# Performance work log

Hardware: AMD Instinct MI355X
Metric: run time of the kernel (lower is better)

## Reference

```python
import jax, jax.numpy as jnp
import numpy as np

V, E, H = 50000, 200, 128
B, R, S, W = 16, 10, 20, 64


def gru_last(x, lengths, Wih, Whh, bih, bhh, reverse=False):
    # x: [N,T,D], lengths: [N] -> final valid hidden state [N,H]
    # Masked-update scan: h only updates on valid timesteps, so after the full
    # scan h equals the packed-sequence final hidden (fwd: t=len-1; bwd: t=0).
    N, T, _ = x.shape
    Hd = Whh.shape[1]
    xi = x @ Wih.T + bih                      # [N,T,3H] input gates, precomputed
    t = jnp.arange(T)
    if reverse:
        xi = xi[:, ::-1]
        valid = (T - 1 - t)[None, :] < lengths[:, None]
    else:
        valid = t[None, :] < lengths[:, None]

    def step(h, inp):
        xg, v = inp
        hg = h @ Whh.T + bhh
        r = jax.nn.sigmoid(xg[:, :Hd] + hg[:, :Hd])
        z = jax.nn.sigmoid(xg[:, Hd:2 * Hd] + hg[:, Hd:2 * Hd])
        n = jnp.tanh(xg[:, 2 * Hd:] + r * hg[:, 2 * Hd:])
        hn = (1.0 - z) * n + z * h
        return jnp.where(v[:, None], hn, h), None

    h0 = jnp.zeros((N, Hd), x.dtype)
    hT, _ = jax.lax.scan(step, h0, (jnp.swapaxes(xi, 0, 1), valid.T))
    return hT


def bigru_last(x, lengths, pf, pb):
    hf = gru_last(x, lengths, *pf, reverse=False)
    hb = gru_last(x, lengths, *pb, reverse=True)
    return 0.5 * (hf + hb)  # reduce bidirectional h_n to hid_dim (mean of dirs)


def setup_inputs() -> dict:
    key = jax.random.key(0)
    ks = jax.random.split(key, 24)

    def gn(k, shape, s=0.1):
        return jax.random.normal(k, shape, dtype=jnp.float32) * s

    return {
        "inputs": jax.random.randint(ks[0], (B, R, S, W), 0, V),
        "sent_lengths": jax.random.randint(ks[1], (B, R, S), 1, W + 1),
        "sent_counts": jax.random.randint(ks[2], (B, R), 1, S + 1),
        "embed": gn(ks[3], (V, E), 1.0),
        "wWih_f": gn(ks[4], (3 * H, E)), "wWhh_f": gn(ks[5], (3 * H, H)),
        "wbih_f": gn(ks[6], (3 * H,)), "wbhh_f": gn(ks[7], (3 * H,)),
        "wWih_b": gn(ks[8], (3 * H, E)), "wWhh_b": gn(ks[9], (3 * H, H)),
        "wbih_b": gn(ks[10], (3 * H,)), "wbhh_b": gn(ks[11], (3 * H,)),
        "sWih_f": gn(ks[12], (3 * H, H)), "sWhh_f": gn(ks[13], (3 * H, H)),
        "sbih_f": gn(ks[14], (3 * H,)), "sbhh_f": gn(ks[15], (3 * H,)),
        "sWih_b": gn(ks[16], (3 * H, H)), "sWhh_b": gn(ks[17], (3 * H, H)),
        "sbih_b": gn(ks[18], (3 * H,)), "sbhh_b": gn(ks[19], (3 * H,)),
        "fc1_w": gn(ks[20], (H // 2, H)), "fc1_b": gn(ks[21], (H // 2,)),
        "fc2_w": gn(ks[22], (1, H // 2)), "fc2_b": gn(ks[23], (1,)),
    }


def reference(inputs, sent_lengths, sent_counts, embed,
              wWih_f, wWhh_f, wbih_f, wbhh_f, wWih_b, wWhh_b, wbih_b, wbhh_b,
              sWih_f, sWhh_f, sbih_f, sbhh_f, sWih_b, sWhh_b, sbih_b, sbhh_b,
              fc1_w, fc1_b, fc2_w, fc2_b):
    b, r, s, w = inputs.shape
    emb = embed[inputs]                                   # [B,R,S,W,E]
    x = emb.reshape(b * r * s, w, -1)
    wlens = sent_lengths.reshape(-1)
    # Word-level BiGRU over all sentences at once (flattened ragged batch)
    sent_rep = bigru_last(x, wlens,
                          (wWih_f, wWhh_f, wbih_f, wbhh_f),
                          (wWih_b, wWhh_b, wbih_b, wbhh_b))  # [B*R*S, H]
    xs = sent_rep.reshape(b * r, s, -1)
    slens = sent_counts.reshape(-1)
    # Sentence-level BiGRU over all reviews at once
    rev = bigru_last(xs, slens,
                     (sWih_f, sWhh_f, sbih_f, sbhh_f),
                     (sWih_b, sWhh_b, sbih_b, sbhh_b)).reshape(b, r, -1)
    h = jax.nn.selu(rev @ fc1_w.T + fc1_b)                # [B,R,H//2]
    r_stars = (h @ fc2_w.T + fc2_b)[..., 0]               # [B,R]
    p_stars = r_stars.mean(-1)                            # [B]
    return p_stars, r_stars
```

## Files before the change

### kernel.cpp

```cpp
#include <hip/hip_runtime.h>
#include <hip/hip_bf16.h>
#include <cstddef>

#define VOCAB 50000
#define EDIM  200
#define HDIM  128
#define BB 16
#define RR 10
#define SS 20
#define WW 64
#define NSENT (BB*RR*SS)
#define NREV  (BB*RR)
#define G3    (3*HDIM)
#define NPROJ (2*G3)

static __device__ __forceinline__ short f2bf(float f) {
    union { float f; unsigned u; } v; v.f = f;
    unsigned r = v.u + 0x7FFFu + ((v.u >> 16) & 1u);
    return (short)(r >> 16);
}
static __device__ __forceinline__ short f2bf_t(float f) {
    union { float f; unsigned u; } v; v.f = f;
    return (short)(v.u >> 16);
}
static __device__ __forceinline__ float bf2f(short s) {
    union { unsigned u; float f; } v;
    v.u = ((unsigned)(unsigned short)s) << 16;
    return v.f;
}
static __device__ __forceinline__ float frcp(float x) {
    return __builtin_amdgcn_rcpf(x);
}
static __device__ __forceinline__ float fsigmoid(float x) {
    return frcp(1.f + __expf(-x));
}
static __device__ __forceinline__ float ftanh(float x) {
    float y = __expf(-2.f * fabsf(x));
    float t = (1.f - y) * frcp(1.f + y);
    return copysignf(t, x);
}

using bf16x8 = __attribute__((ext_vector_type(8))) short;
using f32x4  = __attribute__((ext_vector_type(4))) float;

template<int KREAL, int KPAD>
__global__ __launch_bounds__(256) void preconv(
    const float* __restrict__ A0, int Mreal,
    short* __restrict__ hi, short* __restrict__ lo, int ngroups)
{
    int g = blockIdx.x * 256 + threadIdx.x;
    if (g >= ngroups) return;
    int row = g / (KPAD / 8);
    int k   = (g % (KPAD / 8)) * 8;
    float v[8];
    if (row < Mreal && k < KREAL) {
        const float* p = A0 + (size_t)row * KREAL + k;
        float4 a = *(const float4*)p;
        float4 b = *(const float4*)(p + 4);
        v[0]=a.x; v[1]=a.y; v[2]=a.z; v[3]=a.w;
        v[4]=b.x; v[5]=b.y; v[6]=b.z; v[7]=b.w;
    } else {
        #pragma unroll
        for (int j = 0; j < 8; ++j) v[j] = 0.f;
    }
    bf16x8 h, l;
    #pragma unroll
    for (int j = 0; j < 8; ++j) {
        short t = f2bf_t(v[j]);
        h[j] = t;
        l[j] = f2bf(v[j] - bf2f(t));
    }
    *(bf16x8*)&hi[(size_t)row * KPAD + k] = h;
    *(bf16x8*)&lo[(size_t)row * KPAD + k] = l;
}

#define GM_LDK 40

template<int KREAL, int KPAD, bool AVG>
__global__ __launch_bounds__(256, 2) void gemm_v4(
    const float* __restrict__ A0, const float* __restrict__ A1, int M,
    const short* __restrict__ Bhi_g, const short* __restrict__ Blo_g,
    const float* __restrict__ bias0, const float* __restrict__ bias1,
    float* __restrict__ C)
{
    const int ct = blockIdx.x;
    const int rt = blockIdx.y;
    const int tid = threadIdx.x;
    const int lane = tid & 63;
    const int wid  = tid >> 6;
    const int rlane = lane & 15;
    const int kgrp  = lane >> 4;

    const int rowBase = rt * 128;
    const int colBase = ct * 128;

    __shared__ short Ahi[128][GM_LDK], Alo[128][GM_LDK];
    __shared__ short Bhi[128][GM_LDK], Blo[128][GM_LDK];

    const int wrow = (wid >> 1) * 64;
    const int wcol = (wid & 1) * 64;

    f32x4 acc[4][4];
    #pragma unroll
    for (int i = 0; i < 4; ++i)
        #pragma unroll
        for (int j = 0; j < 4; ++j) acc[i][j] = {0.f, 0.f, 0.f, 0.f};

    const int srow = tid >> 1;
    const int skh  = (tid & 1) << 4;
    const int grow = rowBase + srow;
    const size_t brow = (size_t)(colBase + srow) * KPAD;

    float4 va[4];
    bf16x8 vbh0, vbh1, vbl0, vbl1;

    auto loadA = [&](int k0) {
        #pragma unroll
        for (int i = 0; i < 4; ++i) {
            const int k = k0 + skh + i * 4;
            float4 x = {0.f, 0.f, 0.f, 0.f};
            if (grow < M && k + 3 < KREAL) {
                x = *(const float4*)&A0[(size_t)grow * KREAL + k];
                if (AVG) {
                    float4 y = *(const float4*)&A1[(size_t)grow * KREAL + k];
                    x.x = 0.5f * (x.x + y.x); x.y = 0.5f * (x.y + y.y);
                    x.z = 0.5f * (x.z + y.z); x.w = 0.5f * (x.w + y.w);
                }
            }
            va[i] = x;
        }
    };
    auto loadB = [&](int k0) {
        vbh0 = *(const bf16x8*)&Bhi_g[brow + k0 + skh];
        vbh1 = *(const bf16x8*)&Bhi_g[brow + k0 + skh + 8];
        vbl0 = *(const bf16x8*)&Blo_g[brow + k0 + skh];
        vbl1 = *(const bf16x8*)&Blo_g[brow + k0 + skh + 8];
    };

    loadA(0);
    loadB(0);

    for (int k0 = 0; k0 < KPAD; k0 += 32) {
        {
            float v[16] = {va[0].x, va[0].y, va[0].z, va[0].w,
                           va[1].x, va[1].y, va[1].z, va[1].w,
                           va[2].x, va[2].y, va[2].z, va[2].w,
                           va[3].x, va[3].y, va[3].z, va[3].w};
            bf16x8 h0, h1, l0, l1;
            #pragma unroll
            for (int i = 0; i < 8; ++i) {
                short a = f2bf_t(v[i]);
                h0[i] = a; l0[i] = f2bf(v[i] - bf2f(a));
                short b = f2bf_t(v[i + 8]);
                h1[i] = b; l1[i] = f2bf(v[i + 8] - bf2f(b));
            }
            *(bf16x8*)&Ahi[srow][skh]     = h0;
            *(bf16x8*)&Ahi[srow][skh + 8] = h1;
            *(bf16x8*)&Alo[srow][skh]     = l0;
            *(bf16x8*)&Alo[srow][skh + 8] = l1;
            *(bf16x8*)&Bhi[srow][skh]     = vbh0;
            *(bf16x8*)&Bhi[srow][skh + 8] = vbh1;
            *(bf16x8*)&Blo[srow][skh]     = vbl0;
            *(bf16x8*)&Blo[srow][skh + 8] = vbl1;
        }
        __syncthreads();
        if (k0 + 32 < KPAD) {
            loadA(k0 + 32);
            loadB(k0 + 32);
        }
        bf16x8 ah[4], al[4], bh[4], bl[4];
        #pragma unroll
        for (int mr = 0; mr < 4; ++mr) {
            ah[mr] = *(const bf16x8*)&Ahi[wrow + mr * 16 + rlane][kgrp * 8];
            al[mr] = *(const bf16x8*)&Alo[wrow + mr * 16 + rlane][kgrp * 8];
        }
        #pragma unroll
        for (int nc = 0; nc < 4; ++nc) {
            bh[nc] = *(const bf16x8*)&Bhi[wcol + nc * 16 + rlane][kgrp * 8];
            bl[nc] = *(const bf16x8*)&Blo[wcol + nc * 16 + rlane][kgrp * 8];
        }
        #pragma unroll
        for (int mr = 0; mr < 4; ++mr)
            #pragma unroll
            for (int nc = 0; nc < 4; ++nc) {
                acc[mr][nc] = __builtin_amdgcn_mfma_f32_16x16x32_bf16(
                    ah[mr], bh[nc], acc[mr][nc], 0, 0, 0);
                acc[mr][nc] = __builtin_amdgcn_mfma_f32_16x16x32_bf16(
                    ah[mr], bl[nc], acc[mr][nc], 0, 0, 0);
                acc[mr][nc] = __builtin_amdgcn_mfma_f32_16x16x32_bf16(
                    al[mr], bh[nc], acc[mr][nc], 0, 0, 0);
            }
        __syncthreads();
    }

    const float* bs = (colBase < G3) ? bias0 : bias1;
    const int bcol = (colBase < G3) ? colBase : (colBase - G3);
    #pragma unroll
    for (int nc = 0; nc < 4; ++nc) {
        const int c = wcol + nc * 16 + rlane;
        const float bv = bs[bcol + c];
        #pragma unroll
        for (int mr = 0; mr < 4; ++mr) {
            #pragma unroll
            for (int r = 0; r < 4; ++r) {
                const int grow2 = rowBase + wrow + mr * 16 + kgrp * 4 + r;
                if (grow2 < M)
                    C[(size_t)grow2 * NPROJ + colBase + c] = acc[mr][nc][r] + bv;
            }
        }
    }
}

__global__ __launch_bounds__(256) void sort_all(
    const int* __restrict__ len1, int* __restrict__ order1,
    const int* __restrict__ len2, int* __restrict__ order2)
{
    __shared__ int hist[65];
    const int tid = threadIdx.x;

    for (int i = tid; i < 65; i += 256) hist[i] = 0;
    __syncthreads();
    for (int i = tid; i < NSENT; i += 256) atomicAdd(&hist[len1[i]], 1);
    __syncthreads();
    if (tid == 0) {
        int acc = 0;
        for (int l = 1; l <= WW; ++l) { int c = hist[l]; hist[l] = acc; acc += c; }
    }
    __syncthreads();
    for (int i = tid; i < NSENT; i += 256) {
        int pos = atomicAdd(&hist[len1[i]], 1);
        order1[pos] = i;
    }
    __syncthreads();
    for (int i = tid; i < 65; i += 256) hist[i] = 0;
    __syncthreads();
    for (int i = tid; i < NREV; i += 256) atomicAdd(&hist[len2[i]], 1);
    __syncthreads();
    if (tid == 0) {
        int acc = 0;
        for (int l = 1; l <= SS; ++l) { int c = hist[l]; hist[l] = acc; acc += c; }
    }
    __syncthreads();
    for (int i = tid; i < NREV; i += 256) {
        int pos = atomicAdd(&hist[len2[i]], 1);
        order2[pos] = i;
    }
}

template<bool WORD, int TMAX>
__global__ __launch_bounds__(512, 2) void gru_mfma(
    const float* __restrict__ table,
    const int*   __restrict__ tokens,
    const int*   __restrict__ lengths,
    const int*   __restrict__ order,
    const float* __restrict__ Whh_f, const float* __restrict__ Whh_b,
    const float* __restrict__ bhh_f, const float* __restrict__ bhh_b,
    float* __restrict__ hout_f, float* __restrict__ hout_b,
    int numSeq, int numTiles)
{
    const int dir  = (blockIdx.x >= numTiles) ? 1 : 0;
    const int rawt = dir ? (blockIdx.x - numTiles) : blockIdx.x;
    const int tile = numTiles - 1 - rawt;
    const int base = tile * 16;
    const int tid  = threadIdx.x;
    const int lane = tid & 63;
    const int wid  = tid >> 6;
    const int rlane = lane & 15;
    const int kgrp  = lane >> 4;
    const int e = wid * 16 + rlane;

    __shared__ __align__(16) short sh_hi[2][16][136];
    __shared__ __align__(16) short sh_lo[2][16][136];
    __shared__ int sh_len[16];
    __shared__ int sh_ord[16];
    __shared__ int sh_tok[WORD ? 16 * WW : 1];
    __shared__ int sh_maxlen;

    const float* Whh = dir ? Whh_b : Whh_f;
    const float* bhh = dir ? bhh_b : bhh_f;
    bf16x8 Bhi[3][4], Blo[3][4];
    float bb[3];
    #pragma unroll
    for (int nt = 0; nt < 3; ++nt) {
        const int cb = nt * HDIM + wid * 16;
        const float* wrow = Whh + (size_t)(cb + rlane) * HDIM;
        bb[nt] = bhh[cb + rlane];
        #pragma unroll
        for (int kc = 0; kc < 4; ++kc) {
            const float* wp = wrow + kc * 32 + kgrp * 8;
            float4 w0 = *(const float4*)wp;
            float4 w1 = *(const float4*)(wp + 4);
            float wv[8] = {w0.x, w0.y, w0.z, w0.w, w1.x, w1.y, w1.z, w1.w};
            #pragma unroll
            for (int j = 0; j < 8; ++j) {
                short hi = f2bf_t(wv[j]);
                Bhi[nt][kc][j] = hi;
                Blo[nt][kc][j] = f2bf(wv[j] - bf2f(hi));
            }
        }
    }

    if (tid < 16) {
        int pos = base + tid;
        int seq = (pos < numSeq) ? order[pos] : -1;
        sh_ord[tid] = seq;
        sh_len[tid] = (seq >= 0) ? lengths[seq] : 0;
    }
    __syncthreads();
    if (WORD) {
        for (int f = tid; f < 16 * WW; f += 512) {
            int s = f >> 6;
            int seq = sh_ord[s];
            sh_tok[f] = (seq >= 0) ? tokens[(size_t)seq * WW + (f & 63)] : 0;
        }
    }
    for (int u = tid; u < 2 * 16 * 136; u += 512) {
        ((short*)sh_hi)[u] = 0;
        ((short*)sh_lo)[u] = 0;
    }
    if (tid == 0) {
        int m = 0;
        for (int s = 0; s < 16; ++s) m = max(m, sh_len[s]);
        sh_maxlen = m;
    }
    int lens[4], ords[4];
    #pragma unroll
    for (int j = 0; j < 4; ++j) {
        lens[j] = sh_len[4 * kgrp + j];
        ords[j] = sh_ord[4 * kgrp + j];
    }
    __syncthreads();
    const int maxlen = sh_maxlen;

    auto fetch_xg = [&](int t, float* fr, float* fz, float* fn) {
        #pragma unroll
        for (int j = 0; j < 4; ++j) {
            fr[j] = 0.f; fz[j] = 0.f; fn[j] = 0.f;
            if (t < lens[j]) {
                int tt = dir ? (lens[j] - 1 - t) : t;
                size_t row;
                if (WORD) row = (size_t)sh_tok[(4 * kgrp + j) * WW + tt];
                else      row = (size_t)ords[j] * TMAX + tt;
                const float* xg = table + row * NPROJ + dir * G3 + e;
                fr[j] = xg[0]; fz[j] = xg[HDIM]; fn[j] = xg[2 * HDIM];
            }
        }
    };

    float hold[4] = {0.f, 0.f, 0.f, 0.f};
    float pAr[4], pAz[4], pAn[4];
    float pBr[4], pBz[4], pBn[4];
    fetch_xg(0, pAr, pAz, pAn);
    fetch_xg(1, pBr, pBz, pBn);

#define GRU_STEP(T, PR, PZ, PN)                                               \
    {                                                                         \
        const int cur = (T) & 1, nxt = cur ^ 1;                               \
        bf16x8 ah[4], al[4];                                                  \
        _Pragma("unroll")                                                     \
        for (int kc = 0; kc < 4; ++kc) {                                      \
            ah[kc] = *(const bf16x8*)&sh_hi[cur][rlane][kc * 32 + kgrp * 8];  \
            al[kc] = *(const bf16x8*)&sh_lo[cur][rlane][kc * 32 + kgrp * 8];  \
        }                                                                     \
        f32x4 acc[3];                                                         \
        _Pragma("unroll")                                                     \
        for (int nt = 0; nt < 3; ++nt) {                                      \
            acc[nt] = {0.f, 0.f, 0.f, 0.f};                                   \
            _Pragma("unroll")                                                 \
            for (int kc = 0; kc < 4; ++kc)                                    \
                acc[nt] = __builtin_amdgcn_mfma_f32_16x16x32_bf16(            \
                    ah[kc], Bhi[nt][kc], acc[nt], 0, 0, 0);                   \
            _Pragma("unroll")                                                 \
            for (int kc = 0; kc < 4; ++kc)                                    \
                acc[nt] = __builtin_amdgcn_mfma_f32_16x16x32_bf16(            \
                    ah[kc], Blo[nt][kc], acc[nt], 0, 0, 0);                   \
            _Pragma("unroll")                                                 \
            for (int kc = 0; kc < 4; ++kc)                                    \
                acc[nt] = __builtin_amdgcn_mfma_f32_16x16x32_bf16(            \
                    al[kc], Bhi[nt][kc], acc[nt], 0, 0, 0);                   \
        }                                                                     \
        _Pragma("unroll")                                                     \
        for (int j = 0; j < 4; ++j) {                                         \
            if ((T) < lens[j]) {                                              \
                float hgr = acc[0][j] + bb[0];                                \
                float hgz = acc[1][j] + bb[1];                                \
                float hgn = acc[2][j] + bb[2];                                \
                float rg = fsigmoid(PR[j] + hgr);                             \
                float zg = fsigmoid(PZ[j] + hgz);                             \
                float ng = ftanh(PN[j] + rg * hgn);                           \
                hold[j] = (1.f - zg) * ng + zg * hold[j];                     \
            }                                                                 \
        }                                                                     \
        fetch_xg((T) + 2, PR, PZ, PN);                                        \
        _Pragma("unroll")                                                     \
        for (int j = 0; j < 4; ++j) {                                         \
            const int s = 4 * kgrp + j;                                       \
            short hi = f2bf_t(hold[j]);                                       \
            sh_hi[nxt][s][e] = hi;                                            \
            sh_lo[nxt][s][e] = f2bf(hold[j] - bf2f(hi));                      \
        }                                                                     \
        __syncthreads();                                                      \
    }

    int t = 0;
    for (; t + 1 < maxlen; t += 2) {
        GRU_STEP(t,     pAr, pAz, pAn);
        GRU_STEP(t + 1, pBr, pBz, pBn);
    }
    if (t < maxlen) {
        GRU_STEP(t, pAr, pAz, pAn);
    }
#undef GRU_STEP

    float* hout = dir ? hout_b : hout_f;
    #pragma unroll
    for (int j = 0; j < 4; ++j) {
        if (ords[j] >= 0)
            hout[(size_t)ords[j] * HDIM + e] = hold[j];
    }
}

__global__ __launch_bounds__(64) void head_kernel(
    const float* __restrict__ hsf, const float* __restrict__ hsb,
    const float* __restrict__ fc1_w, const float* __restrict__ fc1_b,
    const float* __restrict__ fc2_w, const float* __restrict__ fc2_b,
    float* __restrict__ out)
{
    const int br = blockIdx.x;
    const int j = threadIdx.x;
    __shared__ float rev[HDIM];
    for (int ee = j; ee < HDIM; ee += 64)
        rev[ee] = 0.5f * (hsf[(size_t)br * HDIM + ee] + hsb[(size_t)br * HDIM + ee]);
    __syncthreads();
    float acc = 0.f;
    #pragma unroll
    for (int k = 0; k < HDIM; ++k)
        acc = fmaf(fc1_w[(size_t)j * HDIM + k], rev[k], acc);
    acc += fc1_b[j];
    const float alpha = 1.6732632423543772f;
    const float scale = 1.0507009873554805f;
    float h1 = scale * (acc > 0.f ? acc : alpha * (expf(acc) - 1.f));
    float contrib = h1 * fc2_w[j];
    #pragma unroll
    for (int off = 32; off > 0; off >>= 1)
        contrib += __shfl_down(contrib, off);
    if (j == 0) out[16 + br] = contrib + fc2_b[0];
}

__global__ void mean_kernel(float* __restrict__ out)
{
    int b = threadIdx.x;
    if (b < BB) {
        float s = 0.f;
        for (int r = 0; r < RR; ++r) s += out[16 + b * RR + r];
        out[b] = s / (float)RR;
    }
}

extern "C" void kernel_launch(void* const* d_in, const int* in_sizes, int n_in,
                              void* d_out, int out_size, void* d_ws, size_t ws_size,
                              hipStream_t stream)
{
    const int*   inputs       = (const int*)d_in[0];
    const int*   sent_lengths = (const int*)d_in[1];
    const int*   sent_counts  = (const int*)d_in[2];
    const float* embed   = (const float*)d_in[3];
    const float* wWih_f  = (const float*)d_in[4];
    const float* wWhh_f  = (const float*)d_in[5];
    const float* wbih_f  = (const float*)d_in[6];
    const float* wbhh_f  = (const float*)d_in[7];
    const float* wWih_b  = (const float*)d_in[8];
    const float* wWhh_b  = (const float*)d_in[9];
    const float* wbih_b  = (const float*)d_in[10];
    const float* wbhh_b  = (const float*)d_in[11];
    const float* sWih_f  = (const float*)d_in[12];
    const float* sWhh_f  = (const float*)d_in[13];
    const float* sbih_f  = (const float*)d_in[14];
    const float* sbhh_f  = (const float*)d_in[15];
    const float* sWih_b  = (const float*)d_in[16];
    const float* sWhh_b  = (const float*)d_in[17];
    const float* sbih_b  = (const float*)d_in[18];
    const float* sbhh_b  = (const float*)d_in[19];
    const float* fc1_w   = (const float*)d_in[20];
    const float* fc1_b   = (const float*)d_in[21];
    const float* fc2_w   = (const float*)d_in[22];
    const float* fc2_b   = (const float*)d_in[23];

    float* ws = (float*)d_ws;
    const size_t projT_elems = (size_t)VOCAB * NPROJ;
    const size_t xgs_elems   = (size_t)NSENT * NPROJ;
    const size_t h_elems     = (size_t)NSENT * HDIM;
    const size_t hs_elems    = (size_t)NREV * HDIM;
    float* projT = ws;
    float* xgs   = projT + projT_elems;
    float* hf    = xgs + xgs_elems;
    float* hb    = hf + h_elems;
    float* hsf   = hb + h_elems;
    float* hsb   = hsf + hs_elems;
    int* order1  = (int*)(hsb + hs_elems);
    int* order2  = order1 + NSENT;
    short* Bw_hi = (short*)(order2 + NREV);
    short* Bw_lo = Bw_hi + 768 * 224;
    short* Sw_hi = Bw_lo + 768 * 224;
    short* Sw_lo = Sw_hi + 768 * 128;

    size_t need = (projT_elems + xgs_elems + 2*h_elems + 2*hs_elems) * sizeof(float)
                + (NSENT + NREV) * sizeof(int)
                + (size_t)(2 * 768 * 224 + 2 * 768 * 128) * sizeof(short);
    if (ws_size < need) return;

    sort_all<<<1, 256, 0, stream>>>(sent_lengths, order1, sent_counts, order2);
    {
        int ng = 384 * 224 / 8;
        preconv<EDIM, 224><<<(ng + 255) / 256, 256, 0, stream>>>(
            wWih_f, 384, Bw_hi, Bw_lo, ng);
        preconv<EDIM, 224><<<(ng + 255) / 256, 256, 0, stream>>>(
            wWih_b, 384, Bw_hi + 384 * 224, Bw_lo + 384 * 224, ng);
    }
    {
        int ng = 384 * 128 / 8;
        preconv<HDIM, HDIM><<<(ng + 255) / 256, 256, 0, stream>>>(
            sWih_f, 384, Sw_hi, Sw_lo, ng);
        preconv<HDIM, HDIM><<<(ng + 255) / 256, 256, 0, stream>>>(
            sWih_b, 384, Sw_hi + 384 * 128, Sw_lo + 384 * 128, ng);
    }

    {
        dim3 grid(NPROJ / 128, (VOCAB + 127) / 128);
        gemm_v4<EDIM, 224, false><<<grid, 256, 0, stream>>>(
            embed, nullptr, VOCAB, Bw_hi, Bw_lo, wbih_f, wbih_b, projT);
    }
    {
        int numTiles = NSENT / 16;
        gru_mfma<true, WW><<<2 * numTiles, 512, 0, stream>>>(
            projT, inputs, sent_lengths, order1,
            wWhh_f, wWhh_b, wbhh_f, wbhh_b,
            hf, hb, NSENT, numTiles);
    }
    {
        dim3 grid(NPROJ / 128, (NSENT + 127) / 128);
        gemm_v4<HDIM, HDIM, true><<<grid, 256, 0, stream>>>(
            hf, hb, NSENT, Sw_hi, Sw_lo, sbih_f, sbih_b, xgs);
    }
    {
        int numTiles = NREV / 16;
        gru_mfma<false, SS><<<2 * numTiles, 512, 0, stream>>>(
            xgs, nullptr, sent_counts, order2,
            sWhh_f, sWhh_b, sbhh_f, sbhh_b,
            hsf, hsb, NREV, numTiles);
    }
    head_kernel<<<NREV, 64, 0, stream>>>(hsf, hsb, fc1_w, fc1_b, fc2_w, fc2_b,
                                         (float*)d_out);
    mean_kernel<<<1, 64, 0, stream>>>((float*)d_out);
}
```

Measured before the change: 299.1 us.

## Stage GEMM epilogue through LDS for coalesced stores, drop register prefetch

The projection GEMM now writes its output tile through shared memory in two halves, so each thread stores contiguous float4 rows instead of scattered scalar stores. The grid is transposed so consecutive blocks walk rows rather than column tiles. The register-level software prefetch of the next K slice is removed, which frees registers but exposes global-load latency before each barrier. Shared memory is merged into one buffer and reused for the epilogue, which adds extra barriers.

```diff
diff --git a/kernel.cpp b/kernel.cpp
--- a/kernel.cpp
+++ b/kernel.cpp
@@ -74,17 +74,15 @@
     *(bf16x8*)&lo[(size_t)row * KPAD + k] = l;
 }
 
-#define GM_LDK 40
-
 template<int KREAL, int KPAD, bool AVG>
-__global__ __launch_bounds__(256, 2) void gemm_v4(
+__global__ __launch_bounds__(256, 2) void gemm_v5(
     const float* __restrict__ A0, const float* __restrict__ A1, int M,
     const short* __restrict__ Bhi_g, const short* __restrict__ Blo_g,
     const float* __restrict__ bias0, const float* __restrict__ bias1,
     float* __restrict__ C)
 {
-    const int ct = blockIdx.x;
-    const int rt = blockIdx.y;
+    const int rt = blockIdx.x;
+    const int ct = blockIdx.y;
     const int tid = threadIdx.x;
     const int lane = tid & 63;
     const int wid  = tid >> 6;
@@ -94,8 +92,11 @@
     const int rowBase = rt * 128;
     const int colBase = ct * 128;
 
-    __shared__ short Ahi[128][GM_LDK], Alo[128][GM_LDK];
-    __shared__ short Bhi[128][GM_LDK], Blo[128][GM_LDK];
+    __shared__ __align__(16) short smem[4 * 128 * 40];
+    short (*Ahi)[40] = (short(*)[40])(smem);
+    short (*Alo)[40] = (short(*)[40])(smem + 5120);
+    short (*Bhi)[40] = (short(*)[40])(smem + 10240);
+    short (*Blo)[40] = (short(*)[40])(smem + 15360);
 
     const int wrow = (wid >> 1) * 64;
     const int wcol = (wid & 1) * 64;
@@ -111,41 +112,23 @@
     const int grow = rowBase + srow;
     const size_t brow = (size_t)(colBase + srow) * KPAD;
 
-    float4 va[4];
-    bf16x8 vbh0, vbh1, vbl0, vbl1;
-
-    auto loadA = [&](int k0) {
-        #pragma unroll
-        for (int i = 0; i < 4; ++i) {
-            const int k = k0 + skh + i * 4;
-            float4 x = {0.f, 0.f, 0.f, 0.f};
-            if (grow < M && k + 3 < KREAL) {
-                x = *(const float4*)&A0[(size_t)grow * KREAL + k];
-                if (AVG) {
-                    float4 y = *(const float4*)&A1[(size_t)grow * KREAL + k];
-                    x.x = 0.5f * (x.x + y.x); x.y = 0.5f * (x.y + y.y);
-                    x.z = 0.5f * (x.z + y.z); x.w = 0.5f * (x.w + y.w);
-                }
-            }
-            va[i] = x;
-        }
-    };
-    auto loadB = [&](int k0) {
-        vbh0 = *(const bf16x8*)&Bhi_g[brow + k0 + skh];
-        vbh1 = *(const bf16x8*)&Bhi_g[brow + k0 + skh + 8];
-        vbl0 = *(const bf16x8*)&Blo_g[brow + k0 + skh];
-        vbl1 = *(const bf16x8*)&Blo_g[brow + k0 + skh + 8];
-    };
-
-    loadA(0);
-    loadB(0);
-
     for (int k0 = 0; k0 < KPAD; k0 += 32) {
         {
-            float v[16] = {va[0].x, va[0].y, va[0].z, va[0].w,
-                           va[1].x, va[1].y, va[1].z, va[1].w,
-                           va[2].x, va[2].y, va[2].z, va[2].w,
-                           va[3].x, va[3].y, va[3].z, va[3].w};
+            float v[16];
+            #pragma unroll
+            for (int i = 0; i < 4; ++i) {
+                const int k = k0 + skh + i * 4;
+                float4 x = {0.f, 0.f, 0.f, 0.f};
+                if (grow < M && k + 3 < KREAL) {
+                    x = *(const float4*)&A0[(size_t)grow * KREAL + k];
+                    if (AVG) {
+                        float4 y = *(const float4*)&A1[(size_t)grow * KREAL + k];
+                        x.x = 0.5f * (x.x + y.x); x.y = 0.5f * (x.y + y.y);
+                        x.z = 0.5f * (x.z + y.z); x.w = 0.5f * (x.w + y.w);
+                    }
+                }
+                v[4*i+0] = x.x; v[4*i+1] = x.y; v[4*i+2] = x.z; v[4*i+3] = x.w;
+            }
             bf16x8 h0, h1, l0, l1;
             #pragma unroll
             for (int i = 0; i < 8; ++i) {
@@ -158,16 +141,12 @@
             *(bf16x8*)&Ahi[srow][skh + 8] = h1;
             *(bf16x8*)&Alo[srow][skh]     = l0;
             *(bf16x8*)&Alo[srow][skh + 8] = l1;
-            *(bf16x8*)&Bhi[srow][skh]     = vbh0;
-            *(bf16x8*)&Bhi[srow][skh + 8] = vbh1;
-            *(bf16x8*)&Blo[srow][skh]     = vbl0;
-            *(bf16x8*)&Blo[srow][skh + 8] = vbl1;
-        }
+        }
+        *(bf16x8*)&Bhi[srow][skh]     = *(const bf16x8*)&Bhi_g[brow + k0 + skh];
+        *(bf16x8*)&Bhi[srow][skh + 8] = *(const bf16x8*)&Bhi_g[brow + k0 + skh + 8];
+        *(bf16x8*)&Blo[srow][skh]     = *(const bf16x8*)&Blo_g[brow + k0 + skh];
+        *(bf16x8*)&Blo[srow][skh + 8] = *(const bf16x8*)&Blo_g[brow + k0 + skh + 8];
         __syncthreads();
-        if (k0 + 32 < KPAD) {
-            loadA(k0 + 32);
-            loadB(k0 + 32);
-        }
         bf16x8 ah[4], al[4], bh[4], bl[4];
         #pragma unroll
         for (int mr = 0; mr < 4; ++mr) {
@@ -195,18 +174,32 @@
 
     const float* bs = (colBase < G3) ? bias0 : bias1;
     const int bcol = (colBase < G3) ? colBase : (colBase - G3);
-    #pragma unroll
-    for (int nc = 0; nc < 4; ++nc) {
-        const int c = wcol + nc * 16 + rlane;
-        const float bv = bs[bcol + c];
-        #pragma unroll
-        for (int mr = 0; mr < 4; ++mr) {
+    float* ldsf = (float*)smem;
+    #pragma unroll
+    for (int half = 0; half < 2; ++half) {
+        __syncthreads();
+        if ((wid & 1) == half) {
             #pragma unroll
-            for (int r = 0; r < 4; ++r) {
-                const int grow2 = rowBase + wrow + mr * 16 + kgrp * 4 + r;
-                if (grow2 < M)
-                    C[(size_t)grow2 * NPROJ + colBase + c] = acc[mr][nc][r] + bv;
+            for (int nc = 0; nc < 4; ++nc) {
+                const int c = nc * 16 + rlane;
+                const float bv = bs[bcol + half * 64 + c];
+                #pragma unroll
+                for (int mr = 0; mr < 4; ++mr)
+                    #pragma unroll
+                    for (int r = 0; r < 4; ++r)
+                        ldsf[(wrow + mr * 16 + kgrp * 4 + r) * 68 + c] =
+                            acc[mr][nc][r] + bv;
             }
+        }
+        __syncthreads();
+        const int row = tid >> 1;
+        const int ch  = (tid & 1) * 32;
+        if (rowBase + row < M) {
+            float* cp = C + (size_t)(rowBase + row) * NPROJ
+                          + colBase + half * 64 + ch;
+            #pragma unroll
+            for (int i = 0; i < 8; ++i)
+                *(float4*)(cp + i * 4) = *(const float4*)&ldsf[row * 68 + ch + i * 4];
         }
     }
 }
@@ -526,8 +519,8 @@
     }
 
     {
-        dim3 grid(NPROJ / 128, (VOCAB + 127) / 128);
-        gemm_v4<EDIM, 224, false><<<grid, 256, 0, stream>>>(
+        dim3 grid((VOCAB + 127) / 128, NPROJ / 128);
+        gemm_v5<EDIM, 224, false><<<grid, 256, 0, stream>>>(
             embed, nullptr, VOCAB, Bw_hi, Bw_lo, wbih_f, wbih_b, projT);
     }
     {
@@ -538,8 +531,8 @@
             hf, hb, NSENT, numTiles);
     }
     {
-        dim3 grid(NPROJ / 128, (NSENT + 127) / 128);
-        gemm_v4<HDIM, HDIM, true><<<grid, 256, 0, stream>>>(
+        dim3 grid((NSENT + 127) / 128, NPROJ / 128);
+        gemm_v5<HDIM, HDIM, true><<<grid, 256, 0, stream>>>(
             hf, hb, NSENT, Sw_hi, Sw_lo, sbih_f, sbih_b, xgs);
     }
     {
```

Result: faster. 286.6 us (-4.2%).
